# Optimization experiments

Hardware: AMD Instinct MI355X
Metric: run time of the kernel (lower is better)

The kernel has to match this reference:

```python
import jax, jax.numpy as jnp
import numpy as np

N_NODES = 50000
N_EDGES = 1_000_000
N_HYPER = 1024
F_IN = 128
F_EDGE = 64


def setup_inputs() -> dict:
    key = jax.random.key(0)
    ks = jax.random.split(key, 20)
    s = 0.05
    return {
        "x": jax.random.normal(ks[0], (N_NODES, F_IN), jnp.float32),
        "edge_index": jax.random.randint(ks[1], (2, N_EDGES), 0, N_NODES, dtype=jnp.int64),
        "edge_weight": jax.random.uniform(ks[2], (N_EDGES,), jnp.float32),
        "edge_features": jax.random.normal(ks[3], (N_HYPER, F_EDGE), jnp.float32),
        "adj_e": jax.random.uniform(ks[4], (N_HYPER, N_HYPER), jnp.float32) / N_HYPER,
        "T": jax.random.uniform(ks[5], (N_NODES, N_HYPER), jnp.float32) / N_HYPER,
        # HypergraphConvLayer 1: 128 -> 64
        "W1": jax.random.normal(ks[6], (F_IN, 64), jnp.float32) * s,
        "b1": jnp.zeros((64,), jnp.float32),
        # HypergraphConvLayer 2: 64 -> 32
        "W2": jax.random.normal(ks[7], (64, 32), jnp.float32) * s,
        "b2": jnp.zeros((32,), jnp.float32),
        # GraphConvolution (CensNet-style): node 32->32, edge 64->32
        "Wn": jax.random.normal(ks[8], (32, 32), jnp.float32) * s,
        "We": jax.random.normal(ks[9], (F_EDGE, 32), jnp.float32) * s,
        "bg": jnp.zeros((32,), jnp.float32),
        # class_classifier: Linear(32,32) -> ReLU -> Linear(32,2) -> Softmax
        "Wc1": jax.random.normal(ks[10], (32, 32), jnp.float32) * s,
        "bc1": jnp.zeros((32,), jnp.float32),
        "Wc2": jax.random.normal(ks[11], (32, 2), jnp.float32) * s,
        "bc2": jnp.zeros((2,), jnp.float32),
    }


def _hconv(h, W, b, src, dst, edge_weight, num_nodes):
    # linear projection then edge-weighted scatter-add: out[dst] += w * h[src]
    h = h @ W + b
    msg = h[src] * edge_weight[:, None]          # [E, d]
    return jax.ops.segment_sum(msg, dst, num_segments=num_nodes)


def reference(x, edge_index, edge_weight, edge_features, adj_e, T,
              W1, b1, W2, b2, Wn, We, bg, Wc1, bc1, Wc2, bc2):
    n = x.shape[0]
    src, dst = edge_index[0], edge_index[1]

    h = jax.nn.relu(_hconv(x, W1, b1, src, dst, edge_weight, n))   # [N,64]
    h = jax.nn.relu(_hconv(h, W2, b2, src, dst, edge_weight, n))   # [N,32]

    # aggregate_node_features: node_features[dst] += h[src]; / num_edges
    num_edges = edge_index.shape[1]
    node_features = jax.ops.segment_sum(h[src], dst, num_segments=n) / num_edges

    # edge_conv: node linear + incidence-weighted hyperedge convolution
    edge_h = adj_e @ (edge_features @ We)                           # [NE,32]
    shared = jax.nn.relu(node_features @ Wn + T @ edge_h + bg)      # [N,32]

    # class_classifier
    c = jax.nn.relu(shared @ Wc1 + bc1)
    logits = c @ Wc2 + bc2
    return jax.nn.softmax(logits, axis=1)                           # [N,2]
```

## Files before the change

### kernel.cpp

```cpp
#include <hip/hip_runtime.h>
#include <hip/hip_fp16.h>

template<int COLS, int K, int RPBT, int OUTH>
__global__ __launch_bounds__(256) void gemm_k(
    const float* __restrict__ X, const float* __restrict__ W,
    const float* __restrict__ bias, void* __restrict__ outp,
    int nrows, float scale, int relu_in)
{
    constexpr int CPT = COLS / 8;
    constexpr int KT  = 32;
    constexpr int NKT = K / KT;
    constexpr int RT  = RPBT / 32;

    __shared__ float sx[RPBT * 36];
    __shared__ float sWT[COLS * 33];

    const int tid = threadIdx.x;
    const int cg  = tid & 7;
    const int rg  = tid >> 3;
    const int r0  = blockIdx.x * RPBT;

    float acc[RT][CPT];
    #pragma unroll
    for (int r = 0; r < RT; ++r)
        #pragma unroll
        for (int c = 0; c < CPT; ++c) acc[r][c] = 0.f;

    for (int kt = 0; kt < NKT; ++kt) {
        #pragma unroll
        for (int j = 0; j < RT; ++j) {
            int i  = tid + j * 256;
            int r  = i >> 3;
            int k4 = i & 7;
            int gr = r0 + r; if (gr >= nrows) gr = nrows - 1;
            float4 v = *(const float4*)&X[(size_t)gr * K + kt * KT + k4 * 4];
            if (relu_in) {
                v.x = fmaxf(v.x, 0.f); v.y = fmaxf(v.y, 0.f);
                v.z = fmaxf(v.z, 0.f); v.w = fmaxf(v.w, 0.f);
            }
            if (scale != 1.f) { v.x *= scale; v.y *= scale; v.z *= scale; v.w *= scale; }
            *(float4*)&sx[r * 36 + k4 * 4] = v;
        }
        for (int i = tid; i < COLS * KT; i += 256) {
            int kl = i / COLS, c = i % COLS;
            sWT[c * 33 + kl] = W[(size_t)(kt * KT + kl) * COLS + c];
        }
        __syncthreads();

        #pragma unroll
        for (int k4 = 0; k4 < 8; ++k4) {
            float4 a[RT];
            #pragma unroll
            for (int r = 0; r < RT; ++r)
                a[r] = *(const float4*)&sx[(r * 32 + rg) * 36 + k4 * 4];
            #pragma unroll
            for (int cc = 0; cc < CPT; ++cc) {
                int c = cg * CPT + cc;
                float w0 = sWT[c * 33 + k4 * 4 + 0];
                float w1 = sWT[c * 33 + k4 * 4 + 1];
                float w2 = sWT[c * 33 + k4 * 4 + 2];
                float w3 = sWT[c * 33 + k4 * 4 + 3];
                #pragma unroll
                for (int r = 0; r < RT; ++r)
                    acc[r][cc] += a[r].x * w0 + a[r].y * w1 + a[r].z * w2 + a[r].w * w3;
            }
        }
        __syncthreads();
    }

    #pragma unroll
    for (int r = 0; r < RT; ++r) {
        int row = r0 + r * 32 + rg;
        if (row < nrows) {
            #pragma unroll
            for (int cc4 = 0; cc4 < CPT / 4; ++cc4) {
                int c = cg * CPT + cc4 * 4;
                float4 o;
                o.x = acc[r][cc4 * 4 + 0] + (bias ? bias[c + 0] : 0.f);
                o.y = acc[r][cc4 * 4 + 1] + (bias ? bias[c + 1] : 0.f);
                o.z = acc[r][cc4 * 4 + 2] + (bias ? bias[c + 2] : 0.f);
                o.w = acc[r][cc4 * 4 + 3] + (bias ? bias[c + 3] : 0.f);
                if constexpr (OUTH) {
                    __half2 h0 = __floats2half2_rn(o.x, o.y);
                    __half2 h1 = __floats2half2_rn(o.z, o.w);
                    uint2 u;
                    u.x = *(unsigned int*)&h0;
                    u.y = *(unsigned int*)&h1;
                    *(uint2*)&((__half*)outp)[(size_t)row * COLS + c] = u;
                } else {
                    *(float4*)&((float*)outp)[(size_t)row * COLS + c] = o;
                }
            }
        }
    }
}

__global__ __launch_bounds__(256, 4) void tgemm2_k(
    const float* __restrict__ T, const float* __restrict__ eh,
    float* __restrict__ par, int nrows)
{
    __shared__ float seh[256 * 32];
    const int tid = threadIdx.x;
    const int ks  = blockIdx.y * 256;

    #pragma unroll
    for (int j = 0; j < 8; ++j) {
        int i = tid + j * 256;
        *(float4*)&seh[i * 4] = *(const float4*)&eh[(size_t)ks * 32 + (size_t)i * 4];
    }
    __syncthreads();

    int row = blockIdx.x * 256 + tid;
    int r   = row < nrows ? row : nrows - 1;
    const float* Tp = T + (size_t)r * 1024 + ks;

    float acc[32];
    #pragma unroll
    for (int c = 0; c < 32; ++c) acc[c] = 0.f;

    float4 t[8];
    #pragma unroll
    for (int q = 0; q < 8; ++q) t[q] = *(const float4*)&Tp[q * 4];

    for (int kc = 0; kc < 8; ++kc) {
        float4 tn[8];
        if (kc < 7) {
            #pragma unroll
            for (int q = 0; q < 8; ++q)
                tn[q] = *(const float4*)&Tp[(kc + 1) * 32 + q * 4];
        }
        #pragma unroll
        for (int q = 0; q < 8; ++q) {
            #pragma unroll
            for (int j = 0; j < 4; ++j) {
                float a = (j == 0) ? t[q].x : (j == 1) ? t[q].y : (j == 2) ? t[q].z : t[q].w;
                int k = kc * 32 + q * 4 + j;
                #pragma unroll
                for (int c4 = 0; c4 < 8; ++c4) {
                    float4 w = *(const float4*)&seh[k * 32 + c4 * 4];
                    acc[c4 * 4 + 0] += a * w.x;
                    acc[c4 * 4 + 1] += a * w.y;
                    acc[c4 * 4 + 2] += a * w.z;
                    acc[c4 * 4 + 3] += a * w.w;
                }
            }
        }
        #pragma unroll
        for (int q = 0; q < 8; ++q) t[q] = tn[q];
    }

    if (row < nrows) {
        float* p = par + (size_t)blockIdx.y * nrows * 32 + (size_t)row * 32;
        #pragma unroll
        for (int c4 = 0; c4 < 8; ++c4)
            *(float4*)&p[c4 * 4] = make_float4(acc[c4 * 4 + 0], acc[c4 * 4 + 1],
                                               acc[c4 * 4 + 2], acc[c4 * 4 + 3]);
    }
}

__global__ __launch_bounds__(256) void classify2_k(
    const float* __restrict__ par, const float* __restrict__ nfacc,
    const float* __restrict__ Wn, const float* __restrict__ bg,
    const float* __restrict__ Wc1, const float* __restrict__ bc1,
    const float* __restrict__ Wc2, const float* __restrict__ bc2,
    float* __restrict__ out, int nrows, float invE)
{
    __shared__ float sWn[1024];
    __shared__ float sWc1T[1024];
    __shared__ float sWc2[64];
    __shared__ float sb[66];

    int tid = threadIdx.x;
    for (int i = tid; i < 1024; i += 256) {
        sWn[i] = Wn[i];
        sWc1T[(i & 31) * 32 + (i >> 5)] = Wc1[i];
    }
    if (tid < 64) sWc2[tid] = Wc2[tid];
    if (tid < 32)      sb[tid] = bc1[tid];
    else if (tid < 64) sb[tid] = bg[tid - 32];
    else if (tid < 66) sb[tid] = bc2[tid - 64];
    __syncthreads();

    int row = blockIdx.x * 256 + tid;
    if (row >= nrows) return;

    float nf[32];
    #pragma unroll
    for (int i4 = 0; i4 < 8; ++i4) {
        float4 v = *(const float4*)&nfacc[(size_t)row * 32 + i4 * 4];
        nf[i4 * 4 + 0] = v.x * invE; nf[i4 * 4 + 1] = v.y * invE;
        nf[i4 * 4 + 2] = v.z * invE; nf[i4 * 4 + 3] = v.w * invE;
    }

    float acc[32];
    #pragma unroll
    for (int c = 0; c < 32; ++c) acc[c] = sb[32 + c];
    #pragma unroll
    for (int k = 0; k < 32; ++k) {
        float a = nf[k];
        #pragma unroll
        for (int c4 = 0; c4 < 8; ++c4) {
            float4 w = *(const float4*)&sWn[k * 32 + c4 * 4];
            acc[c4 * 4 + 0] += a * w.x;
            acc[c4 * 4 + 1] += a * w.y;
            acc[c4 * 4 + 2] += a * w.z;
            acc[c4 * 4 + 3] += a * w.w;
        }
    }

    size_t stride = (size_t)nrows * 32;
    #pragma unroll
    for (int i4 = 0; i4 < 8; ++i4) {
        const float* base = par + (size_t)row * 32 + i4 * 4;
        float4 v0 = *(const float4*)(base);
        float4 v1 = *(const float4*)(base + stride);
        float4 v2 = *(const float4*)(base + 2 * stride);
        float4 v3 = *(const float4*)(base + 3 * stride);
        acc[i4 * 4 + 0] = fmaxf(acc[i4 * 4 + 0] + v0.x + v1.x + v2.x + v3.x, 0.f);
        acc[i4 * 4 + 1] = fmaxf(acc[i4 * 4 + 1] + v0.y + v1.y + v2.y + v3.y, 0.f);
        acc[i4 * 4 + 2] = fmaxf(acc[i4 * 4 + 2] + v0.z + v1.z + v2.z + v3.z, 0.f);
        acc[i4 * 4 + 3] = fmaxf(acc[i4 * 4 + 3] + v0.w + v1.w + v2.w + v3.w, 0.f);
    }

    float l0 = sb[64], l1 = sb[65];
    #pragma unroll
    for (int jj = 0; jj < 32; ++jj) {
        float s = sb[jj];
        #pragma unroll
        for (int k4 = 0; k4 < 8; ++k4) {
            float4 w4 = *(const float4*)&sWc1T[jj * 32 + k4 * 4];
            s += acc[k4 * 4 + 0] * w4.x + acc[k4 * 4 + 1] * w4.y
               + acc[k4 * 4 + 2] * w4.z + acc[k4 * 4 + 3] * w4.w;
        }
        s = fmaxf(s, 0.f);
        l0 += s * sWc2[jj * 2 + 0];
        l1 += s * sWc2[jj * 2 + 1];
    }
    float p0 = 1.f / (1.f + expf(l1 - l0));
    float p1 = 1.f / (1.f + expf(l0 - l1));
    *(float2*)&out[(size_t)row * 2] = make_float2(p0, p1);
}

__global__ void hist_k(const int* __restrict__ dst, int* __restrict__ deg, int E)
{
    int e = blockIdx.x * 256 + threadIdx.x;
    if (e < E) atomicAdd(&deg[dst[e]], 1);
}

__global__ void scan1_k(const int* __restrict__ deg, int* __restrict__ bsum, int N)
{
    __shared__ int s[256];
    int t = threadIdx.x, i = blockIdx.x * 256 + t;
    s[t] = (i < N) ? deg[i] : 0;
    __syncthreads();
    for (int off = 128; off > 0; off >>= 1) {
        if (t < off) s[t] += s[t + off];
        __syncthreads();
    }
    if (t == 0) bsum[blockIdx.x] = s[0];
}

__global__ void scan2_k(const int* __restrict__ bsum, int* __restrict__ boff,
                        int NB, int* __restrict__ rsN)
{
    __shared__ int s[256];
    int t = threadIdx.x;
    int v = (t < NB) ? bsum[t] : 0;
    s[t] = v;
    __syncthreads();
    for (int off = 1; off < 256; off <<= 1) {
        int u = (t >= off) ? s[t - off] : 0;
        __syncthreads();
        s[t] += u;
        __syncthreads();
    }
    if (t < NB) boff[t] = s[t] - v;
    if (t == NB - 1) *rsN = s[t];
}

__global__ void scan3_k(const int* __restrict__ deg, const int* __restrict__ boff,
                        int* __restrict__ rs, int* __restrict__ cur, int N)
{
    __shared__ int s[256];
    int t = threadIdx.x, i = blockIdx.x * 256 + t;
    int v = (i < N) ? deg[i] : 0;
    s[t] = v;
    __syncthreads();
    for (int off = 1; off < 256; off <<= 1) {
        int u = (t >= off) ? s[t - off] : 0;
        __syncthreads();
        s[t] += u;
        __syncthreads();
    }
    if (i < N) {
        int ex = boff[blockIdx.x] + s[t] - v;
        rs[i] = ex;
        cur[i] = ex;
    }
}

__global__ void fill_k(const int* __restrict__ src, const int* __restrict__ dst,
                       const float* __restrict__ ew, int* __restrict__ cur,
                       int2* __restrict__ epk, int E)
{
    int e = blockIdx.x * 256 + threadIdx.x;
    if (e < E) {
        int pos = atomicAdd(&cur[dst[e]], 1);
        epk[pos] = make_int2(src[e], __float_as_int(ew[e]));
    }
}

__global__ __launch_bounds__(256) void gather64h_k(
    const __half* __restrict__ hp, const int2* __restrict__ epk,
    const int* __restrict__ rs, float* __restrict__ outv, int N)
{
    int wid  = (blockIdx.x * 256 + threadIdx.x) >> 6;
    if (wid >= N) return;
    int lane = threadIdx.x & 63;
    int e4   = lane >> 4;
    int ch   = lane & 15;
    int j0 = rs[wid], j1 = rs[wid + 1];

    float4 acc = make_float4(0.f, 0.f, 0.f, 0.f);
    for (int j = j0 + e4; j < j1; j += 4) {
        int2 e = epk[j];
        float w = __int_as_float(e.y);
        uint2 u = *(const uint2*)&hp[(size_t)e.x * 64 + ch * 4];
        float2 a = __half22float2(*(__half2*)&u.x);
        float2 b = __half22float2(*(__half2*)&u.y);
        acc.x += a.x * w; acc.y += a.y * w;
        acc.z += b.x * w; acc.w += b.y * w;
    }
    #pragma unroll
    for (int off = 16; off < 64; off <<= 1) {
        acc.x += __shfl_xor(acc.x, off);
        acc.y += __shfl_xor(acc.y, off);
        acc.z += __shfl_xor(acc.z, off);
        acc.w += __shfl_xor(acc.w, off);
    }
    if (e4 == 0)
        *(float4*)&outv[(size_t)wid * 64 + ch * 4] = acc;
}

__global__ __launch_bounds__(256) void gather32h_wr_k(
    const __half* __restrict__ hp, const int2* __restrict__ epk,
    const int* __restrict__ rs, __half* __restrict__ outh, int N)
{
    int wid  = (blockIdx.x * 256 + threadIdx.x) >> 6;
    if (wid >= N) return;
    int lane = threadIdx.x & 63;
    int e8   = lane >> 3;
    int ch   = lane & 7;
    int j0 = rs[wid], j1 = rs[wid + 1];

    float4 acc = make_float4(0.f, 0.f, 0.f, 0.f);
    for (int j = j0 + e8; j < j1; j += 8) {
        int2 e = epk[j];
        float w = __int_as_float(e.y);
        uint2 u = *(const uint2*)&hp[(size_t)e.x * 32 + ch * 4];
        float2 a = __half22float2(*(__half2*)&u.x);
        float2 b = __half22float2(*(__half2*)&u.y);
        acc.x += a.x * w; acc.y += a.y * w;
        acc.z += b.x * w; acc.w += b.y * w;
    }
    #pragma unroll
    for (int off = 8; off < 64; off <<= 1) {
        acc.x += __shfl_xor(acc.x, off);
        acc.y += __shfl_xor(acc.y, off);
        acc.z += __shfl_xor(acc.z, off);
        acc.w += __shfl_xor(acc.w, off);
    }
    if (e8 == 0) {
        __half2 h0 = __floats2half2_rn(fmaxf(acc.x, 0.f), fmaxf(acc.y, 0.f));
        __half2 h1 = __floats2half2_rn(fmaxf(acc.z, 0.f), fmaxf(acc.w, 0.f));
        uint2 u;
        u.x = *(unsigned int*)&h0;
        u.y = *(unsigned int*)&h1;
        *(uint2*)&outh[(size_t)wid * 32 + ch * 4] = u;
    }
}

__global__ __launch_bounds__(256) void gather32h_uf_k(
    const __half* __restrict__ hp, const int2* __restrict__ epk,
    const int* __restrict__ rs, float* __restrict__ outv, int N)
{
    int wid  = (blockIdx.x * 256 + threadIdx.x) >> 6;
    if (wid >= N) return;
    int lane = threadIdx.x & 63;
    int e8   = lane >> 3;
    int ch   = lane & 7;
    int j0 = rs[wid], j1 = rs[wid + 1];

    float4 acc = make_float4(0.f, 0.f, 0.f, 0.f);
    for (int j = j0 + e8; j < j1; j += 8) {
        int2 e = epk[j];
        uint2 u = *(const uint2*)&hp[(size_t)e.x * 32 + ch * 4];
        float2 a = __half22float2(*(__half2*)&u.x);
        float2 b = __half22float2(*(__half2*)&u.y);
        acc.x += a.x; acc.y += a.y;
        acc.z += b.x; acc.w += b.y;
    }
    #pragma unroll
    for (int off = 8; off < 64; off <<= 1) {
        acc.x += __shfl_xor(acc.x, off);
        acc.y += __shfl_xor(acc.y, off);
        acc.z += __shfl_xor(acc.z, off);
        acc.w += __shfl_xor(acc.w, off);
    }
    if (e8 == 0)
        *(float4*)&outv[(size_t)wid * 32 + ch * 4] = acc;
}

__global__ void efwe_k(const float* __restrict__ ef, const float* __restrict__ We,
                       float* __restrict__ tmp)
{
    int idx = blockIdx.x * 256 + threadIdx.x;
    int row = idx >> 5, c = idx & 31;
    float s = 0.f;
    #pragma unroll
    for (int k = 0; k < 64; ++k)
        s += ef[row * 64 + k] * We[k * 32 + c];
    tmp[row * 32 + c] = s;
}

__global__ void adjmm_k(const float* __restrict__ adj, const float* __restrict__ tmp,
                        float* __restrict__ edge_h)
{
    int kq     = blockIdx.x & 3;
    int rowblk = blockIdx.x >> 2;
    int r = rowblk * 8 + (threadIdx.x >> 5);
    int c = threadIdx.x & 31;
    float s = 0.f;
    int k0 = kq * 256;
    #pragma unroll 8
    for (int k = k0; k < k0 + 256; ++k)
        s += adj[r * 1024 + k] * tmp[k * 32 + c];
    atomicAdd(&edge_h[r * 32 + c], s);
}

extern "C" void kernel_launch(void* const* d_in, const int* in_sizes, int n_in,
                              void* d_out, int out_size, void* d_ws, size_t ws_size,
                              hipStream_t stream)
{
    const float* x   = (const float*)d_in[0];
    const int*   ei  = (const int*)  d_in[1];
    const float* ew  = (const float*)d_in[2];
    const float* ef  = (const float*)d_in[3];
    const float* adj = (const float*)d_in[4];
    const float* T   = (const float*)d_in[5];
    const float* W1  = (const float*)d_in[6];
    const float* b1  = (const float*)d_in[7];
    const float* W2  = (const float*)d_in[8];
    const float* b2  = (const float*)d_in[9];
    const float* Wn  = (const float*)d_in[10];
    const float* We  = (const float*)d_in[11];
    const float* bg  = (const float*)d_in[12];
    const float* Wc1 = (const float*)d_in[13];
    const float* bc1 = (const float*)d_in[14];
    const float* Wc2 = (const float*)d_in[15];
    const float* bc2 = (const float*)d_in[16];
    float* out = (float*)d_out;

    const int N = in_sizes[0] / 128;
    const int E = in_sizes[1] / 2;
    const int* srcIdx = ei;
    const int* dstIdx = ei + E;

    float* ws = (float*)d_ws;
    size_t o = 0;
    float*  h1acc  = ws + o; o += (size_t)N * 64;
    float*  nfacc  = ws + o; o += (size_t)N * 32;
    float*  edge_h = ws + o; o += 1024 * 32;
    float*  tmp    = ws + o; o += 1024 * 32;
    float*  par    = ws + o; o += (size_t)N * 128;
    __half* h1p_h  = (__half*)(ws + o); o += (size_t)N * 32;
    __half* h2p_h  = (__half*)(ws + o); o += (size_t)N * 16;
    __half* h2r_h  = (__half*)(ws + o); o += (size_t)N * 16;
    int2*   epk    = (int2*)(ws + o);   o += (size_t)E * 2;
    int*    deg    = (int*)(ws + o);    o += N;
    int*    rs     = (int*)(ws + o);    o += N + 1;
    int*    cur    = (int*)(ws + o);    o += N + 1;
    int*    bsum   = (int*)(ws + o);    o += 256;
    int*    boff   = (int*)(ws + o);    o += 256;

    const int NB  = (N + 255) / 256;
    const int NBG = (N + 63) / 64;
    const int NBW = (N * 64 + 255) / 256;

    (void)hipMemsetAsync(deg, 0, (size_t)N * sizeof(int), stream);
    (void)hipMemsetAsync(edge_h, 0, 1024 * 32 * sizeof(float), stream);

    gemm_k<64, 128, 64, 1><<<NBG, 256, 0, stream>>>(x, W1, b1, h1p_h, N, 1.f, 0);

    hist_k<<<(E + 255) / 256, 256, 0, stream>>>(dstIdx, deg, E);
    scan1_k<<<NB, 256, 0, stream>>>(deg, bsum, N);
    scan2_k<<<1, 256, 0, stream>>>(bsum, boff, NB, rs + N);
    scan3_k<<<NB, 256, 0, stream>>>(deg, boff, rs, cur, N);
    fill_k<<<(E + 255) / 256, 256, 0, stream>>>(srcIdx, dstIdx, ew, cur, epk, E);

    gather64h_k<<<NBW, 256, 0, stream>>>(h1p_h, epk, rs, h1acc, N);

    gemm_k<32, 64, 64, 1><<<NBG, 256, 0, stream>>>(h1acc, W2, b2, h2p_h, N, 1.f, 1);

    gather32h_wr_k<<<NBW, 256, 0, stream>>>(h2p_h, epk, rs, h2r_h, N);

    gather32h_uf_k<<<NBW, 256, 0, stream>>>(h2r_h, epk, rs, nfacc, N);

    efwe_k<<<128, 256, 0, stream>>>(ef, We, tmp);
    adjmm_k<<<512, 256, 0, stream>>>(adj, tmp, edge_h);

    tgemm2_k<<<dim3(NB, 4), 256, 0, stream>>>(T, edge_h, par, N);

    classify2_k<<<NB, 256, 0, stream>>>(par, nfacc, Wn, bg, Wc1, bc1, Wc2, bc2,
                                        out, N, 1.f / (float)E);
}
```

Before: 687.5 us.

## Fuse T-GEMM with classifier, single-block scan, drop split-K in adj matmul

Merges the T@edge_h GEMM and the classifier into one kernel that loads the full 1024x32 edge_h into shared memory, which removes the partial-sum buffer and its round trip. The three-kernel prefix scan becomes one 1024-thread block, and the adj matmul drops split-K atomics and the memset. In exchange, the fused kernel uses about 136KB of LDS per block with only ~196 blocks, which reduces occupancy and parallelism for streaming the 200MB T matrix.

New measurement: 810.9 us. 17.9% more time.

```diff
diff --git a/kernel.cpp b/kernel.cpp
--- a/kernel.cpp
+++ b/kernel.cpp
@@ -95,36 +95,68 @@
     }
 }
 
-__global__ __launch_bounds__(256, 4) void tgemm2_k(
+__global__ __launch_bounds__(256) void tgc_k(
     const float* __restrict__ T, const float* __restrict__ eh,
-    float* __restrict__ par, int nrows)
-{
-    __shared__ float seh[256 * 32];
+    const float* __restrict__ nfacc, const float* __restrict__ Wn,
+    const float* __restrict__ bg, const float* __restrict__ Wc1,
+    const float* __restrict__ bc1, const float* __restrict__ Wc2,
+    const float* __restrict__ bc2, float* __restrict__ out,
+    int nrows, float invE)
+{
+    __shared__ float seh[1024 * 32];
+    __shared__ float sWn[1024];
+    __shared__ float sWc1T[1024];
+    __shared__ float sWc2[64];
+    __shared__ float sb[66];
+
     const int tid = threadIdx.x;
-    const int ks  = blockIdx.y * 256;
-
-    #pragma unroll
-    for (int j = 0; j < 8; ++j) {
+    #pragma unroll
+    for (int j = 0; j < 32; ++j) {
         int i = tid + j * 256;
-        *(float4*)&seh[i * 4] = *(const float4*)&eh[(size_t)ks * 32 + (size_t)i * 4];
-    }
+        *(float4*)&seh[i * 4] = *(const float4*)&eh[(size_t)i * 4];
+    }
+    for (int i = tid; i < 1024; i += 256) {
+        sWn[i] = Wn[i];
+        sWc1T[(i & 31) * 32 + (i >> 5)] = Wc1[i];
+    }
+    if (tid < 64) sWc2[tid] = Wc2[tid];
+    if (tid < 32)      sb[tid] = bc1[tid];
+    else if (tid < 64) sb[tid] = bg[tid - 32];
+    else if (tid < 66) sb[tid] = bc2[tid - 64];
     __syncthreads();
 
     int row = blockIdx.x * 256 + tid;
     int r   = row < nrows ? row : nrows - 1;
-    const float* Tp = T + (size_t)r * 1024 + ks;
+    const float* Tp = T + (size_t)r * 1024;
 
     float acc[32];
     #pragma unroll
-    for (int c = 0; c < 32; ++c) acc[c] = 0.f;
+    for (int c = 0; c < 32; ++c) acc[c] = sb[32 + c];
+    #pragma unroll
+    for (int k4 = 0; k4 < 8; ++k4) {
+        float4 v = *(const float4*)&nfacc[(size_t)r * 32 + k4 * 4];
+        float a[4] = { v.x * invE, v.y * invE, v.z * invE, v.w * invE };
+        #pragma unroll
+        for (int j = 0; j < 4; ++j) {
+            int k = k4 * 4 + j;
+            #pragma unroll
+            for (int c4 = 0; c4 < 8; ++c4) {
+                float4 w = *(const float4*)&sWn[k * 32 + c4 * 4];
+                acc[c4 * 4 + 0] += a[j] * w.x;
+                acc[c4 * 4 + 1] += a[j] * w.y;
+                acc[c4 * 4 + 2] += a[j] * w.z;
+                acc[c4 * 4 + 3] += a[j] * w.w;
+            }
+        }
+    }
 
     float4 t[8];
     #pragma unroll
     for (int q = 0; q < 8; ++q) t[q] = *(const float4*)&Tp[q * 4];
 
-    for (int kc = 0; kc < 8; ++kc) {
+    for (int kc = 0; kc < 32; ++kc) {
         float4 tn[8];
-        if (kc < 7) {
+        if (kc < 31) {
             #pragma unroll
             for (int q = 0; q < 8; ++q)
                 tn[q] = *(const float4*)&Tp[(kc + 1) * 32 + q * 4];
@@ -149,88 +181,20 @@
         for (int q = 0; q < 8; ++q) t[q] = tn[q];
     }
 
-    if (row < nrows) {
-        float* p = par + (size_t)blockIdx.y * nrows * 32 + (size_t)row * 32;
-        #pragma unroll
-        for (int c4 = 0; c4 < 8; ++c4)
-            *(float4*)&p[c4 * 4] = make_float4(acc[c4 * 4 + 0], acc[c4 * 4 + 1],
-                                               acc[c4 * 4 + 2], acc[c4 * 4 + 3]);
-    }
-}
-
-__global__ __launch_bounds__(256) void classify2_k(
-    const float* __restrict__ par, const float* __restrict__ nfacc,
-    const float* __restrict__ Wn, const float* __restrict__ bg,
-    const float* __restrict__ Wc1, const float* __restrict__ bc1,
-    const float* __restrict__ Wc2, const float* __restrict__ bc2,
-    float* __restrict__ out, int nrows, float invE)
-{
-    __shared__ float sWn[1024];
-    __shared__ float sWc1T[1024];
-    __shared__ float sWc2[64];
-    __shared__ float sb[66];
-
-    int tid = threadIdx.x;
-    for (int i = tid; i < 1024; i += 256) {
-        sWn[i] = Wn[i];
-        sWc1T[(i & 31) * 32 + (i >> 5)] = Wc1[i];
-    }
-    if (tid < 64) sWc2[tid] = Wc2[tid];
-    if (tid < 32)      sb[tid] = bc1[tid];
-    else if (tid < 64) sb[tid] = bg[tid - 32];
-    else if (tid < 66) sb[tid] = bc2[tid - 64];
-    __syncthreads();
-
-    int row = blockIdx.x * 256 + tid;
     if (row >= nrows) return;
 
-    float nf[32];
-    #pragma unroll
-    for (int i4 = 0; i4 < 8; ++i4) {
-        float4 v = *(const float4*)&nfacc[(size_t)row * 32 + i4 * 4];
-        nf[i4 * 4 + 0] = v.x * invE; nf[i4 * 4 + 1] = v.y * invE;
-        nf[i4 * 4 + 2] = v.z * invE; nf[i4 * 4 + 3] = v.w * invE;
-    }
-
-    float acc[32];
-    #pragma unroll
-    for (int c = 0; c < 32; ++c) acc[c] = sb[32 + c];
-    #pragma unroll
-    for (int k = 0; k < 32; ++k) {
-        float a = nf[k];
-        #pragma unroll
-        for (int c4 = 0; c4 < 8; ++c4) {
-            float4 w = *(const float4*)&sWn[k * 32 + c4 * 4];
-            acc[c4 * 4 + 0] += a * w.x;
-            acc[c4 * 4 + 1] += a * w.y;
-            acc[c4 * 4 + 2] += a * w.z;
-            acc[c4 * 4 + 3] += a * w.w;
-        }
-    }
-
-    size_t stride = (size_t)nrows * 32;
-    #pragma unroll
-    for (int i4 = 0; i4 < 8; ++i4) {
-        const float* base = par + (size_t)row * 32 + i4 * 4;
-        float4 v0 = *(const float4*)(base);
-        float4 v1 = *(const float4*)(base + stride);
-        float4 v2 = *(const float4*)(base + 2 * stride);
-        float4 v3 = *(const float4*)(base + 3 * stride);
-        acc[i4 * 4 + 0] = fmaxf(acc[i4 * 4 + 0] + v0.x + v1.x + v2.x + v3.x, 0.f);
-        acc[i4 * 4 + 1] = fmaxf(acc[i4 * 4 + 1] + v0.y + v1.y + v2.y + v3.y, 0.f);
-        acc[i4 * 4 + 2] = fmaxf(acc[i4 * 4 + 2] + v0.z + v1.z + v2.z + v3.z, 0.f);
-        acc[i4 * 4 + 3] = fmaxf(acc[i4 * 4 + 3] + v0.w + v1.w + v2.w + v3.w, 0.f);
-    }
+    #pragma unroll
+    for (int c = 0; c < 32; ++c) acc[c] = fmaxf(acc[c], 0.f);
 
     float l0 = sb[64], l1 = sb[65];
     #pragma unroll
     for (int jj = 0; jj < 32; ++jj) {
         float s = sb[jj];
         #pragma unroll
-        for (int k4 = 0; k4 < 8; ++k4) {
-            float4 w4 = *(const float4*)&sWc1T[jj * 32 + k4 * 4];
-            s += acc[k4 * 4 + 0] * w4.x + acc[k4 * 4 + 1] * w4.y
-               + acc[k4 * 4 + 2] * w4.z + acc[k4 * 4 + 3] * w4.w;
+        for (int c4 = 0; c4 < 8; ++c4) {
+            float4 w4 = *(const float4*)&sWc1T[jj * 32 + c4 * 4];
+            s += acc[c4 * 4 + 0] * w4.x + acc[c4 * 4 + 1] * w4.y
+               + acc[c4 * 4 + 2] * w4.z + acc[c4 * 4 + 3] * w4.w;
         }
         s = fmaxf(s, 0.f);
         l0 += s * sWc2[jj * 2 + 0];
@@ -247,56 +211,33 @@
     if (e < E) atomicAdd(&deg[dst[e]], 1);
 }
 
-__global__ void scan1_k(const int* __restrict__ deg, int* __restrict__ bsum, int N)
-{
-    __shared__ int s[256];
-    int t = threadIdx.x, i = blockIdx.x * 256 + t;
-    s[t] = (i < N) ? deg[i] : 0;
+__global__ __launch_bounds__(1024) void scanall_k(
+    const int* __restrict__ deg, int* __restrict__ rs, int* __restrict__ cur, int N)
+{
+    __shared__ int part[1024];
+    const int t  = threadIdx.x;
+    const int CH = (N + 1023) >> 10;
+    int lo = t * CH, hi = lo + CH;
+    if (lo > N) lo = N;
+    if (hi > N) hi = N;
+
+    int s = 0;
+    for (int i = lo; i < hi; ++i) s += deg[i];
+    part[t] = s;
     __syncthreads();
-    for (int off = 128; off > 0; off >>= 1) {
-        if (t < off) s[t] += s[t + off];
+    for (int off = 1; off < 1024; off <<= 1) {
+        int u = (t >= off) ? part[t - off] : 0;
         __syncthreads();
-    }
-    if (t == 0) bsum[blockIdx.x] = s[0];
-}
-
-__global__ void scan2_k(const int* __restrict__ bsum, int* __restrict__ boff,
-                        int NB, int* __restrict__ rsN)
-{
-    __shared__ int s[256];
-    int t = threadIdx.x;
-    int v = (t < NB) ? bsum[t] : 0;
-    s[t] = v;
-    __syncthreads();
-    for (int off = 1; off < 256; off <<= 1) {
-        int u = (t >= off) ? s[t - off] : 0;
+        part[t] += u;
         __syncthreads();
-        s[t] += u;
-        __syncthreads();
-    }
-    if (t < NB) boff[t] = s[t] - v;
-    if (t == NB - 1) *rsN = s[t];
-}
-
-__global__ void scan3_k(const int* __restrict__ deg, const int* __restrict__ boff,
-                        int* __restrict__ rs, int* __restrict__ cur, int N)
-{
-    __shared__ int s[256];
-    int t = threadIdx.x, i = blockIdx.x * 256 + t;
-    int v = (i < N) ? deg[i] : 0;
-    s[t] = v;
-    __syncthreads();
-    for (int off = 1; off < 256; off <<= 1) {
-        int u = (t >= off) ? s[t - off] : 0;
-        __syncthreads();
-        s[t] += u;
-        __syncthreads();
-    }
-    if (i < N) {
-        int ex = boff[blockIdx.x] + s[t] - v;
-        rs[i] = ex;
+    }
+    int ex = part[t] - s;
+    for (int i = lo; i < hi; ++i) {
+        rs[i]  = ex;
         cur[i] = ex;
-    }
+        ex += deg[i];
+    }
+    if (t == 1023) rs[N] = part[1023];
 }
 
 __global__ void fill_k(const int* __restrict__ src, const int* __restrict__ dst,
@@ -423,19 +364,16 @@
     tmp[row * 32 + c] = s;
 }
 
-__global__ void adjmm_k(const float* __restrict__ adj, const float* __restrict__ tmp,
-                        float* __restrict__ edge_h)
-{
-    int kq     = blockIdx.x & 3;
-    int rowblk = blockIdx.x >> 2;
-    int r = rowblk * 8 + (threadIdx.x >> 5);
+__global__ void adjmm2_k(const float* __restrict__ adj, const float* __restrict__ tmp,
+                         float* __restrict__ edge_h)
+{
+    int r = blockIdx.x * 8 + (threadIdx.x >> 5);
     int c = threadIdx.x & 31;
     float s = 0.f;
-    int k0 = kq * 256;
     #pragma unroll 8
-    for (int k = k0; k < k0 + 256; ++k)
+    for (int k = 0; k < 1024; ++k)
         s += adj[r * 1024 + k] * tmp[k * 32 + c];
-    atomicAdd(&edge_h[r * 32 + c], s);
+    edge_h[r * 32 + c] = s;
 }
 
 extern "C" void kernel_launch(void* const* d_in, const int* in_sizes, int n_in,
@@ -472,7 +410,6 @@
     float*  nfacc  = ws + o; o += (size_t)N * 32;
     float*  edge_h = ws + o; o += 1024 * 32;
     float*  tmp    = ws + o; o += 1024 * 32;
-    float*  par    = ws + o; o += (size_t)N * 128;
     __half* h1p_h  = (__half*)(ws + o); o += (size_t)N * 32;
     __half* h2p_h  = (__half*)(ws + o); o += (size_t)N * 16;
     __half* h2r_h  = (__half*)(ws + o); o += (size_t)N * 16;
@@ -480,22 +417,17 @@
     int*    deg    = (int*)(ws + o);    o += N;
     int*    rs     = (int*)(ws + o);    o += N + 1;
     int*    cur    = (int*)(ws + o);    o += N + 1;
-    int*    bsum   = (int*)(ws + o);    o += 256;
-    int*    boff   = (int*)(ws + o);    o += 256;
 
     const int NB  = (N + 255) / 256;
     const int NBG = (N + 63) / 64;
     const int NBW = (N * 64 + 255) / 256;
 
     (void)hipMemsetAsync(deg, 0, (size_t)N * sizeof(int), stream);
-    (void)hipMemsetAsync(edge_h, 0, 1024 * 32 * sizeof(float), stream);
 
     gemm_k<64, 128, 64, 1><<<NBG, 256, 0, stream>>>(x, W1, b1, h1p_h, N, 1.f, 0);
 
     hist_k<<<(E + 255) / 256, 256, 0, stream>>>(dstIdx, deg, E);
-    scan1_k<<<NB, 256, 0, stream>>>(deg, bsum, N);
-    scan2_k<<<1, 256, 0, stream>>>(bsum, boff, NB, rs + N);
-    scan3_k<<<NB, 256, 0, stream>>>(deg, boff, rs, cur, N);
+    scanall_k<<<1, 1024, 0, stream>>>(deg, rs, cur, N);
     fill_k<<<(E + 255) / 256, 256, 0, stream>>>(srcIdx, dstIdx, ew, cur, epk, E);
 
     gather64h_k<<<NBW, 256, 0, stream>>>(h1p_h, epk, rs, h1acc, N);
@@ -507,10 +439,8 @@
     gather32h_uf_k<<<NBW, 256, 0, stream>>>(h2r_h, epk, rs, nfacc, N);
 
     efwe_k<<<128, 256, 0, stream>>>(ef, We, tmp);
-    adjmm_k<<<512, 256, 0, stream>>>(adj, tmp, edge_h);
-
-    tgemm2_k<<<dim3(NB, 4), 256, 0, stream>>>(T, edge_h, par, N);
-
-    classify2_k<<<NB, 256, 0, stream>>>(par, nfacc, Wn, bg, Wc1, bc1, Wc2, bc2,
-                                        out, N, 1.f / (float)E);
-}
+    adjmm2_k<<<128, 256, 0, stream>>>(adj, tmp, edge_h);
+
+    tgc_k<<<NB, 256, 0, stream>>>(T, edge_h, nfacc, Wn, bg, Wc1, bc1, Wc2, bc2,
+                                  out, N, 1.f / (float)E);
+}
```
